# Kernel tuning notes

Hardware: AMD Instinct MI355X
Metric: run time of the kernel (lower is better)

## Reference

```python
import jax, jax.numpy as jnp
import numpy as np

N_H = 256
N_LAYERS = 3
D_IN = 2  # concat([t, x], axis=1)


def setup_inputs() -> dict:
    key = jax.random.key(0)
    ks = jax.random.split(key, 20)
    N = 131072
    H, L = N_H, N_LAYERS

    def xavier(k, shape):
        fan_in, fan_out = shape[-2], shape[-1]
        limit = np.sqrt(6.0 / (fan_in + fan_out)).astype(np.float32)
        return jax.random.uniform(k, shape, jnp.float32, -limit, limit)

    inp = {
        "t": jax.random.uniform(ks[0], (N, 1), jnp.float32),
        "x": jax.random.normal(ks[1], (N, 1), jnp.float32),
        # initial dense layer: [2, H]
        "W0": xavier(ks[2], (D_IN, H)),
        "b0": jnp.zeros((1, H), jnp.float32),
        # stacked per-layer LSTM-like weights: U* [L, 2, H], W* [L, H, H], b* [L, 1, H]
        "Uz": xavier(ks[3], (L, D_IN, H)),
        "Ug": xavier(ks[4], (L, D_IN, H)),
        "Ur": xavier(ks[5], (L, D_IN, H)),
        "Uh": xavier(ks[6], (L, D_IN, H)),
        "Wz": xavier(ks[7], (L, H, H)),
        "Wg": xavier(ks[8], (L, H, H)),
        "Wr": xavier(ks[9], (L, H, H)),
        "Wh": xavier(ks[10], (L, H, H)),
        "bz": jnp.zeros((L, 1, H), jnp.float32),
        "bg": jnp.zeros((L, 1, H), jnp.float32),
        "br": jnp.zeros((L, 1, H), jnp.float32),
        "bh": jnp.zeros((L, 1, H), jnp.float32),
        # final dense layer: [H, 1]
        "Wf": xavier(ks[11], (H, 1)),
        "bf": jnp.zeros((1, 1), jnp.float32),
    }
    return inp


def _dgm_forward(t, x, W0, b0, Uz, Ug, Ur, Uh, Wz, Wg, Wr, Wh, bz, bg, br, bh, Wf, bf):
    X = jnp.concatenate([t, x], axis=1)            # [N, 2]
    S1 = jnp.tanh(X @ W0 + b0)                     # [N, H] -- initial state, held fixed

    def layer_step(S, params):
        uz, ug, ur, uh, wz, wg, wr, wh, pz, pg, pr, ph = params
        Z = jnp.tanh(X @ uz + S @ wz + pz)
        G = jnp.tanh(X @ ug + S1 @ wg + pg)
        R = jnp.tanh(X @ ur + S @ wr + pr)
        Hg = jnp.tanh(X @ uh + (S * R) @ wh + ph)
        Snew = (1.0 - G) * Hg + Z * S
        return Snew, None

    S, _ = jax.lax.scan(layer_step, S1, (Uz, Ug, Ur, Uh, Wz, Wg, Wr, Wh, bz, bg, br, bh))
    return S @ Wf + bf                             # [N, 1]


def reference(t, x, W0, b0, Uz, Ug, Ur, Uh, Wz, Wg, Wr, Wh, bz, bg, br, bh, Wf, bf):
    return _dgm_forward(t, x, W0, b0, Uz, Ug, Ur, Uh, Wz, Wg, Wr, Wh, bz, bg, br, bh, Wf, bf)
```

## Files before the change

kernel.cpp:

```cpp
#include <hip/hip_runtime.h>


typedef __attribute__((ext_vector_type(8))) short bf16x8;
typedef __attribute__((ext_vector_type(4))) float f32x4;

#if __has_builtin(__builtin_amdgcn_exp2f)
#define EXP2F(x) __builtin_amdgcn_exp2f(x)
#else
#define EXP2F(x) __expf((x) * 0.6931471805599453f)
#endif

__device__ __forceinline__ short f2bf(float f) {
    unsigned u = __float_as_uint(f);
    unsigned r = (u + 0x7FFFu + ((u >> 16) & 1u)) >> 16;
    return (short)r;
}
__device__ __forceinline__ float bf2f(short h) {
    return __uint_as_float(((unsigned)(unsigned short)h) << 16);
}
__device__ __forceinline__ unsigned cvtpk(float lo, float hi) {
    unsigned r;
    asm("v_cvt_pk_bf16_f32 %0, %1, %2" : "=v"(r) : "v"(lo), "v"(hi));
    return r;
}
__device__ __forceinline__ float rcp_1pe2x(float x) {
    float e = EXP2F(x * 2.8853900817779268f);
    return __builtin_amdgcn_rcpf(e + 1.0f);
}
__device__ __forceinline__ float fast_tanh(float x) {
    return fmaf(-2.0f, rcp_1pe2x(x), 1.0f);
}
__device__ __forceinline__ int sw_off(int r, int k) {
    return r * 256 + ((((k >> 3) ^ r) & 31) << 3) + (k & 7);
}
__device__ __forceinline__ unsigned pk2(float a, float b) { return cvtpk(a, b); }
__device__ __forceinline__ float upk(unsigned p, int hi) {
    return __uint_as_float(hi ? (p & 0xFFFF0000u) : (p << 16));
}

__global__ void pack_w(const float* __restrict__ Wz, const float* __restrict__ Wg,
                       const float* __restrict__ Wr, const float* __restrict__ Wh,
                       short* __restrict__ out) {
    int idx = blockIdx.x * 256 + threadIdx.x;
    int mat = idx >> 16;
    int e   = idx & 65535;
    int l = mat >> 2, g = mat & 3;
    int i  = e & 7;
    int ln = (e >> 3) & 63;
    int kb = (e >> 9) & 7;
    int c  = e >> 12;
    int k = kb * 32 + (ln >> 4) * 8 + i;
    int n = c * 16 + (ln & 15);
    const float* W = (g == 0) ? Wz : (g == 1) ? Wg : (g == 2) ? Wr : Wh;
    out[idx] = f2bf(W[l * 65536 + k * 256 + n]);
}

__device__ __forceinline__ void gate_gemm(const short* __restrict__ In,
                                          const short* __restrict__ Wm,
                                          const float* __restrict__ U,
                                          const float* __restrict__ bias,
                                          const float2* __restrict__ txS,
                                          int q, int c15, int w,
                                          f32x4 acc[2][2]) {
    float2 tx[8];
#pragma unroll
    for (int rb = 0; rb < 2; rb++)
#pragma unroll
        for (int ii = 0; ii < 4; ii++) tx[rb * 4 + ii] = txS[rb * 16 + q * 4 + ii];
#pragma unroll
    for (int cb = 0; cb < 2; cb++) {
        int col = (w * 2 + cb) * 16 + c15;
        float u0 = U[col], u1 = U[256 + col], bb = bias[col];
#pragma unroll
        for (int rb = 0; rb < 2; rb++)
#pragma unroll
            for (int ii = 0; ii < 4; ii++)
                acc[rb][cb][ii] = bb + tx[rb * 4 + ii].x * u0 + tx[rb * 4 + ii].y * u1;
    }
    __builtin_amdgcn_s_setprio(1);
#pragma unroll
    for (int kb = 0; kb < 8; kb++) {
        bf16x8 a[2];
#pragma unroll
        for (int rb = 0; rb < 2; rb++) {
            int r = rb * 16 + c15;
            a[rb] = *(const bf16x8*)(In + r * 256 + ((((kb * 4 + q) ^ r) & 31) << 3));
        }
#pragma unroll
        for (int cb = 0; cb < 2; cb++) {
            bf16x8 b = *(const bf16x8*)(Wm + ((((w * 2 + cb) * 8 + kb) * 64 + (q * 16 + c15)) << 3));
#pragma unroll
            for (int rb = 0; rb < 2; rb++)
                acc[rb][cb] = __builtin_amdgcn_mfma_f32_16x16x32_bf16(a[rb], b, acc[rb][cb], 0, 0, 0);
        }
    }
    __builtin_amdgcn_s_setprio(0);
}

__global__ __launch_bounds__(512, 4)
void dgm_main(const float* __restrict__ T, const float* __restrict__ X,
              const float* __restrict__ W0, const float* __restrict__ b0,
              const float* __restrict__ Uz, const float* __restrict__ Ug,
              const float* __restrict__ Ur, const float* __restrict__ Uh,
              const float* __restrict__ bz, const float* __restrict__ bg,
              const float* __restrict__ br, const float* __restrict__ bh,
              const float* __restrict__ Wf, const float* __restrict__ bfp,
              const short* __restrict__ Wp, float* __restrict__ out) {
    __shared__ __align__(16) short Sb[8192];
    __shared__ __align__(16) short S1b[8192];
    __shared__ float2 txS[32];

    const int tid = threadIdx.x;
    const int w   = tid >> 6;
    const int ln  = tid & 63;
    const int q   = ln >> 4;
    const int c15 = ln & 15;
    const int m0  = blockIdx.x * 32;

    if (tid < 32) txS[tid] = make_float2(T[m0 + tid], X[m0 + tid]);
    __syncthreads();

    {
        int col  = tid & 255;
        int half = tid >> 8;
        float w00 = W0[col], w01 = W0[256 + col], bb = b0[col];
#pragma unroll 4
        for (int rr = 0; rr < 16; rr++) {
            int r = half * 16 + rr;
            float2 tx = txS[r];
            short v = f2bf(fast_tanh(tx.x * w00 + tx.y * w01 + bb));
            int off = sw_off(r, col);
            S1b[off] = v;
            Sb[off]  = v;
        }
    }
    __syncthreads();

    unsigned sreg[2][2][2];
#pragma unroll
    for (int rb = 0; rb < 2; rb++)
#pragma unroll
        for (int cb = 0; cb < 2; cb++) {
            int col = (w * 2 + cb) * 16 + c15;
#pragma unroll
            for (int p = 0; p < 2; p++) {
                unsigned lo = (unsigned short)Sb[sw_off(rb * 16 + q * 4 + 2 * p,     col)];
                unsigned hi = (unsigned short)Sb[sw_off(rb * 16 + q * 4 + 2 * p + 1, col)];
                sreg[rb][cb][p] = lo | (hi << 16);
            }
        }

    for (int l = 0; l < 3; l++) {
        const short* Wzp = Wp + (l * 4 + 0) * 65536;
        const short* Wgp = Wp + (l * 4 + 1) * 65536;
        const short* Wrp = Wp + (l * 4 + 2) * 65536;
        const short* Whp = Wp + (l * 4 + 3) * 65536;

        f32x4 acc[2][2];
        unsigned zsp[2][2][2], srp[2][2][2], gmp[2][2][2];

        gate_gemm(Sb, Wzp, Uz + l * 512, bz + l * 256, txS, q, c15, w, acc);
#pragma unroll
        for (int rb = 0; rb < 2; rb++)
#pragma unroll
            for (int cb = 0; cb < 2; cb++)
#pragma unroll
                for (int p = 0; p < 2; p++)
                    zsp[rb][cb][p] = pk2(
                        fast_tanh(acc[rb][cb][2 * p])     * upk(sreg[rb][cb][p], 0),
                        fast_tanh(acc[rb][cb][2 * p + 1]) * upk(sreg[rb][cb][p], 1));

        gate_gemm(Sb, Wrp, Ur + l * 512, br + l * 256, txS, q, c15, w, acc);
#pragma unroll
        for (int rb = 0; rb < 2; rb++)
#pragma unroll
            for (int cb = 0; cb < 2; cb++)
#pragma unroll
                for (int p = 0; p < 2; p++)
                    srp[rb][cb][p] = pk2(
                        upk(sreg[rb][cb][p], 0) * fast_tanh(acc[rb][cb][2 * p]),
                        upk(sreg[rb][cb][p], 1) * fast_tanh(acc[rb][cb][2 * p + 1]));

        gate_gemm(S1b, Wgp, Ug + l * 512, bg + l * 256, txS, q, c15, w, acc);
#pragma unroll
        for (int rb = 0; rb < 2; rb++)
#pragma unroll
            for (int cb = 0; cb < 2; cb++)
#pragma unroll
                for (int p = 0; p < 2; p++)
                    gmp[rb][cb][p] = pk2(2.0f * rcp_1pe2x(acc[rb][cb][2 * p]),
                                         2.0f * rcp_1pe2x(acc[rb][cb][2 * p + 1]));

        __syncthreads();
#pragma unroll
        for (int rb = 0; rb < 2; rb++)
#pragma unroll
            for (int cb = 0; cb < 2; cb++) {
                int col = (w * 2 + cb) * 16 + c15;
#pragma unroll
                for (int p = 0; p < 2; p++) {
                    Sb[sw_off(rb * 16 + q * 4 + 2 * p,     col)] = (short)(srp[rb][cb][p] & 0xFFFFu);
                    Sb[sw_off(rb * 16 + q * 4 + 2 * p + 1, col)] = (short)(srp[rb][cb][p] >> 16);
                }
            }
        __syncthreads();

        gate_gemm(Sb, Whp, Uh + l * 512, bh + l * 256, txS, q, c15, w, acc);

#pragma unroll
        for (int rb = 0; rb < 2; rb++)
#pragma unroll
            for (int cb = 0; cb < 2; cb++)
#pragma unroll
                for (int p = 0; p < 2; p++) {
                    float sn0 = fmaf(upk(gmp[rb][cb][p], 0),
                                     fast_tanh(acc[rb][cb][2 * p]),
                                     upk(zsp[rb][cb][p], 0));
                    float sn1 = fmaf(upk(gmp[rb][cb][p], 1),
                                     fast_tanh(acc[rb][cb][2 * p + 1]),
                                     upk(zsp[rb][cb][p], 1));
                    srp[rb][cb][p] = pk2(sn0, sn1);
                }

        __syncthreads();
#pragma unroll
        for (int rb = 0; rb < 2; rb++)
#pragma unroll
            for (int cb = 0; cb < 2; cb++) {
                int col = (w * 2 + cb) * 16 + c15;
#pragma unroll
                for (int p = 0; p < 2; p++) {
                    Sb[sw_off(rb * 16 + q * 4 + 2 * p,     col)] = (short)(srp[rb][cb][p] & 0xFFFFu);
                    Sb[sw_off(rb * 16 + q * 4 + 2 * p + 1, col)] = (short)(srp[rb][cb][p] >> 16);
                    sreg[rb][cb][p] = srp[rb][cb][p];
                }
            }
        __syncthreads();
    }

    {
        int row = tid >> 4;
        int seg = tid & 15;
        float sum = 0.0f;
#pragma unroll
        for (int j = 0; j < 2; j++) {
            int ch = seg * 2 + j;
            bf16x8 sv = *(const bf16x8*)(Sb + row * 256 + (((ch ^ row) & 31) << 3));
            float4 wa = *(const float4*)(Wf + ch * 8);
            float4 wb = *(const float4*)(Wf + ch * 8 + 4);
            sum += bf2f(sv[0]) * wa.x + bf2f(sv[1]) * wa.y + bf2f(sv[2]) * wa.z + bf2f(sv[3]) * wa.w
                 + bf2f(sv[4]) * wb.x + bf2f(sv[5]) * wb.y + bf2f(sv[6]) * wb.z + bf2f(sv[7]) * wb.w;
        }
        sum += __shfl_down(sum, 8, 16);
        sum += __shfl_down(sum, 4, 16);
        sum += __shfl_down(sum, 2, 16);
        sum += __shfl_down(sum, 1, 16);
        if (seg == 0) out[m0 + row] = sum + bfp[0];
    }
}

extern "C" void kernel_launch(void* const* d_in, const int* in_sizes, int n_in,
                              void* d_out, int out_size, void* d_ws, size_t ws_size,
                              hipStream_t stream) {
    const float* T  = (const float*)d_in[0];
    const float* X  = (const float*)d_in[1];
    const float* W0 = (const float*)d_in[2];
    const float* b0 = (const float*)d_in[3];
    const float* Uz = (const float*)d_in[4];
    const float* Ug = (const float*)d_in[5];
    const float* Ur = (const float*)d_in[6];
    const float* Uh = (const float*)d_in[7];
    const float* Wz = (const float*)d_in[8];
    const float* Wg = (const float*)d_in[9];
    const float* Wr = (const float*)d_in[10];
    const float* Wh = (const float*)d_in[11];
    const float* bz = (const float*)d_in[12];
    const float* bg = (const float*)d_in[13];
    const float* br = (const float*)d_in[14];
    const float* bh = (const float*)d_in[15];
    const float* Wf = (const float*)d_in[16];
    const float* bfp= (const float*)d_in[17];
    float* out = (float*)d_out;
    short* Wp = (short*)d_ws;
    const int N = in_sizes[0];

    pack_w<<<(12 * 65536) / 256, 256, 0, stream>>>(Wz, Wg, Wr, Wh, Wp);
    dgm_main<<<N / 32, 512, 0, stream>>>(T, X, W0, b0, Uz, Ug, Ur, Uh,
                                         bz, bg, br, bh, Wf, bfp, Wp, out);
}
```

Baseline: 408.9 us.

## Fold input projection and bias into an extra MFMA and prescale weights by 2log2e

The per-gate X@U + bias term is now computed by one extra bf16 MFMA per column block, using a padded [t, x, 1, 0...] activation tile in shared memory and packed U/bias weights, instead of scalar FMAs from global U/bias loads. All weights, U and biases are prescaled by 2*log2(e) when packed, so the tanh/sigmoid helper skips a multiply per element. This cuts VALU work and global scalar loads per gate. In exchange, U, bias, t and x are rounded to bf16 (a precision risk), the kernel uses extra LDS and workspace, and a small pack kernel is added.

After: 416.2 us. About the same (+1.8%).

```diff
diff --git a/kernel.cpp b/kernel.cpp
--- a/kernel.cpp
+++ b/kernel.cpp
@@ -10,6 +10,8 @@
 #define EXP2F(x) __expf((x) * 0.6931471805599453f)
 #endif
 
+#define C2LOG2E 2.8853900817779268f
+
 __device__ __forceinline__ short f2bf(float f) {
     unsigned u = __float_as_uint(f);
     unsigned r = (u + 0x7FFFu + ((u >> 16) & 1u)) >> 16;
@@ -23,12 +25,12 @@
     asm("v_cvt_pk_bf16_f32 %0, %1, %2" : "=v"(r) : "v"(lo), "v"(hi));
     return r;
 }
-__device__ __forceinline__ float rcp_1pe2x(float x) {
-    float e = EXP2F(x * 2.8853900817779268f);
+__device__ __forceinline__ float rcp_e1(float sacc) {
+    float e = EXP2F(sacc);
     return __builtin_amdgcn_rcpf(e + 1.0f);
 }
-__device__ __forceinline__ float fast_tanh(float x) {
-    return fmaf(-2.0f, rcp_1pe2x(x), 1.0f);
+__device__ __forceinline__ float tanh_s(float sacc) {
+    return fmaf(-2.0f, rcp_e1(sacc), 1.0f);
 }
 __device__ __forceinline__ int sw_off(int r, int k) {
     return r * 256 + ((((k >> 3) ^ r) & 31) << 3) + (k & 7);
@@ -52,32 +54,51 @@
     int k = kb * 32 + (ln >> 4) * 8 + i;
     int n = c * 16 + (ln & 15);
     const float* W = (g == 0) ? Wz : (g == 1) ? Wg : (g == 2) ? Wr : Wh;
-    out[idx] = f2bf(W[l * 65536 + k * 256 + n]);
+    out[idx] = f2bf(W[l * 65536 + k * 256 + n] * C2LOG2E);
+}
+
+__global__ void pack_ue(const float* __restrict__ Uz, const float* __restrict__ Ug,
+                        const float* __restrict__ Ur, const float* __restrict__ Uh,
+                        const float* __restrict__ bz, const float* __restrict__ bg,
+                        const float* __restrict__ br, const float* __restrict__ bh,
+                        short* __restrict__ out) {
+    int e = blockIdx.x * 256 + threadIdx.x;
+    int mat = e >> 13;
+    int r   = e & 8191;
+    int i    = r & 7;
+    int ln   = (r >> 3) & 63;
+    int cblk = r >> 9;
+    int k = (ln >> 4) * 8 + i;
+    int n = cblk * 16 + (ln & 15);
+    int l = mat >> 2, g = mat & 3;
+    const float* U = (g == 0) ? Uz : (g == 1) ? Ug : (g == 2) ? Ur : Uh;
+    const float* B = (g == 0) ? bz : (g == 1) ? bg : (g == 2) ? br : bh;
+    float v = (k == 0) ? U[l * 512 + n]
+            : (k == 1) ? U[l * 512 + 256 + n]
+            : (k == 2) ? B[l * 256 + n]
+            : 0.0f;
+    out[e] = f2bf(v * C2LOG2E);
 }
 
 __device__ __forceinline__ void gate_gemm(const short* __restrict__ In,
                                           const short* __restrict__ Wm,
-                                          const float* __restrict__ U,
-                                          const float* __restrict__ bias,
-                                          const float2* __restrict__ txS,
+                                          const short* __restrict__ Ue,
+                                          const short* __restrict__ Xe,
                                           int q, int c15, int w,
                                           f32x4 acc[2][2]) {
-    float2 tx[8];
+    bf16x8 ax[2];
 #pragma unroll
     for (int rb = 0; rb < 2; rb++)
-#pragma unroll
-        for (int ii = 0; ii < 4; ii++) tx[rb * 4 + ii] = txS[rb * 16 + q * 4 + ii];
+        ax[rb] = *(const bf16x8*)(Xe + (rb * 16 + c15) * 40 + q * 8);
+    __builtin_amdgcn_s_setprio(1);
 #pragma unroll
     for (int cb = 0; cb < 2; cb++) {
-        int col = (w * 2 + cb) * 16 + c15;
-        float u0 = U[col], u1 = U[256 + col], bb = bias[col];
-#pragma unroll
-        for (int rb = 0; rb < 2; rb++)
-#pragma unroll
-            for (int ii = 0; ii < 4; ii++)
-                acc[rb][cb][ii] = bb + tx[rb * 4 + ii].x * u0 + tx[rb * 4 + ii].y * u1;
-    }
-    __builtin_amdgcn_s_setprio(1);
+        bf16x8 bu = *(const bf16x8*)(Ue + (((w * 2 + cb) * 64 + (q * 16 + c15)) << 3));
+        f32x4 z = {0.0f, 0.0f, 0.0f, 0.0f};
+#pragma unroll
+        for (int rb = 0; rb < 2; rb++)
+            acc[rb][cb] = __builtin_amdgcn_mfma_f32_16x16x32_bf16(ax[rb], bu, z, 0, 0, 0);
+    }
 #pragma unroll
     for (int kb = 0; kb < 8; kb++) {
         bf16x8 a[2];
@@ -100,14 +121,11 @@
 __global__ __launch_bounds__(512, 4)
 void dgm_main(const float* __restrict__ T, const float* __restrict__ X,
               const float* __restrict__ W0, const float* __restrict__ b0,
-              const float* __restrict__ Uz, const float* __restrict__ Ug,
-              const float* __restrict__ Ur, const float* __restrict__ Uh,
-              const float* __restrict__ bz, const float* __restrict__ bg,
-              const float* __restrict__ br, const float* __restrict__ bh,
               const float* __restrict__ Wf, const float* __restrict__ bfp,
               const short* __restrict__ Wp, float* __restrict__ out) {
     __shared__ __align__(16) short Sb[8192];
     __shared__ __align__(16) short S1b[8192];
+    __shared__ __align__(16) short XeS[1280];
     __shared__ float2 txS[32];
 
     const int tid = threadIdx.x;
@@ -120,15 +138,27 @@
     if (tid < 32) txS[tid] = make_float2(T[m0 + tid], X[m0 + tid]);
     __syncthreads();
 
+#pragma unroll
+    for (int e = tid; e < 1024; e += 512) {
+        int r = e >> 5, k = e & 31;
+        float2 t2 = txS[r];
+        short v = (k == 0) ? f2bf(t2.x)
+                : (k == 1) ? f2bf(t2.y)
+                : (k == 2) ? (short)0x3F80
+                : (short)0;
+        XeS[r * 40 + k] = v;
+    }
+
     {
         int col  = tid & 255;
         int half = tid >> 8;
-        float w00 = W0[col], w01 = W0[256 + col], bb = b0[col];
+        float w00 = W0[col] * C2LOG2E, w01 = W0[256 + col] * C2LOG2E;
+        float bb  = b0[col] * C2LOG2E;
 #pragma unroll 4
         for (int rr = 0; rr < 16; rr++) {
             int r = half * 16 + rr;
             float2 tx = txS[r];
-            short v = f2bf(fast_tanh(tx.x * w00 + tx.y * w01 + bb));
+            short v = f2bf(tanh_s(tx.x * w00 + tx.y * w01 + bb));
             int off = sw_off(r, col);
             S1b[off] = v;
             Sb[off]  = v;
@@ -150,16 +180,21 @@
             }
         }
 
+    const short* Uep = Wp + 12 * 65536;
     for (int l = 0; l < 3; l++) {
         const short* Wzp = Wp + (l * 4 + 0) * 65536;
         const short* Wgp = Wp + (l * 4 + 1) * 65536;
         const short* Wrp = Wp + (l * 4 + 2) * 65536;
         const short* Whp = Wp + (l * 4 + 3) * 65536;
+        const short* Uzp = Uep + (l * 4 + 0) * 8192;
+        const short* Ugp = Uep + (l * 4 + 1) * 8192;
+        const short* Urp = Uep + (l * 4 + 2) * 8192;
+        const short* Uhp = Uep + (l * 4 + 3) * 8192;
 
         f32x4 acc[2][2];
         unsigned zsp[2][2][2], srp[2][2][2], gmp[2][2][2];
 
-        gate_gemm(Sb, Wzp, Uz + l * 512, bz + l * 256, txS, q, c15, w, acc);
+        gate_gemm(Sb, Wzp, Uzp, XeS, q, c15, w, acc);
 #pragma unroll
         for (int rb = 0; rb < 2; rb++)
 #pragma unroll
@@ -167,10 +202,10 @@
 #pragma unroll
                 for (int p = 0; p < 2; p++)
                     zsp[rb][cb][p] = pk2(
-                        fast_tanh(acc[rb][cb][2 * p])     * upk(sreg[rb][cb][p], 0),
-                        fast_tanh(acc[rb][cb][2 * p + 1]) * upk(sreg[rb][cb][p], 1));
-
-        gate_gemm(Sb, Wrp, Ur + l * 512, br + l * 256, txS, q, c15, w, acc);
+                        tanh_s(acc[rb][cb][2 * p])     * upk(sreg[rb][cb][p], 0),
+                        tanh_s(acc[rb][cb][2 * p + 1]) * upk(sreg[rb][cb][p], 1));
+
+        gate_gemm(Sb, Wrp, Urp, XeS, q, c15, w, acc);
 #pragma unroll
         for (int rb = 0; rb < 2; rb++)
 #pragma unroll
@@ -178,18 +213,18 @@
 #pragma unroll
                 for (int p = 0; p < 2; p++)
                     srp[rb][cb][p] = pk2(
-                        upk(sreg[rb][cb][p], 0) * fast_tanh(acc[rb][cb][2 * p]),
-                        upk(sreg[rb][cb][p], 1) * fast_tanh(acc[rb][cb][2 * p + 1]));
-
-        gate_gemm(S1b, Wgp, Ug + l * 512, bg + l * 256, txS, q, c15, w, acc);
+                        upk(sreg[rb][cb][p], 0) * tanh_s(acc[rb][cb][2 * p]),
+                        upk(sreg[rb][cb][p], 1) * tanh_s(acc[rb][cb][2 * p + 1]));
+
+        gate_gemm(S1b, Wgp, Ugp, XeS, q, c15, w, acc);
 #pragma unroll
         for (int rb = 0; rb < 2; rb++)
 #pragma unroll
             for (int cb = 0; cb < 2; cb++)
 #pragma unroll
                 for (int p = 0; p < 2; p++)
-                    gmp[rb][cb][p] = pk2(2.0f * rcp_1pe2x(acc[rb][cb][2 * p]),
-                                         2.0f * rcp_1pe2x(acc[rb][cb][2 * p + 1]));
+                    gmp[rb][cb][p] = pk2(2.0f * rcp_e1(acc[rb][cb][2 * p]),
+                                         2.0f * rcp_e1(acc[rb][cb][2 * p + 1]));
 
         __syncthreads();
 #pragma unroll
@@ -205,7 +240,7 @@
             }
         __syncthreads();
 
-        gate_gemm(Sb, Whp, Uh + l * 512, bh + l * 256, txS, q, c15, w, acc);
+        gate_gemm(Sb, Whp, Uhp, XeS, q, c15, w, acc);
 
 #pragma unroll
         for (int rb = 0; rb < 2; rb++)
@@ -214,10 +249,10 @@
 #pragma unroll
                 for (int p = 0; p < 2; p++) {
                     float sn0 = fmaf(upk(gmp[rb][cb][p], 0),
-                                     fast_tanh(acc[rb][cb][2 * p]),
+                                     tanh_s(acc[rb][cb][2 * p]),
                                      upk(zsp[rb][cb][p], 0));
                     float sn1 = fmaf(upk(gmp[rb][cb][p], 1),
-                                     fast_tanh(acc[rb][cb][2 * p + 1]),
+                                     tanh_s(acc[rb][cb][2 * p + 1]),
                                      upk(zsp[rb][cb][p], 1));
                     srp[rb][cb][p] = pk2(sn0, sn1);
                 }
@@ -285,6 +320,7 @@
     const int N = in_sizes[0];
 
     pack_w<<<(12 * 65536) / 256, 256, 0, stream>>>(Wz, Wg, Wr, Wh, Wp);
-    dgm_main<<<N / 32, 512, 0, stream>>>(T, X, W0, b0, Uz, Ug, Ur, Uh,
-                                         bz, bg, br, bh, Wf, bfp, Wp, out);
-}
+    pack_ue<<<(12 * 8192) / 256, 256, 0, stream>>>(Uz, Ug, Ur, Uh, bz, bg, br, bh,
+                                                   Wp + 12 * 65536);
+    dgm_main<<<N / 32, 512, 0, stream>>>(T, X, W0, b0, Wf, bfp, Wp, out);
+}
```
